# Optimization experiments

Measured on AMD Instinct MI355X. Metric: run time of the kernel, lower is better.

Reference implementation:

```python
import jax, jax.numpy as jnp
import numpy as np

CODE_DIMS = [32, 32, 16]   # prod = 16384 out features
FEAT_DIM = 1024
EPS = 1e-6


def setup_inputs() -> dict:
    key = jax.random.key(0)
    kx, kw = jax.random.split(key)
    x = jax.random.normal(kx, (4, 2048, FEAT_DIM), dtype=jnp.float32)
    # per-chunk trunc-normal init like _init_weights: std = sqrt(2/(feat_dim+code_dim)), clipped at +-3 std
    parts = []
    for i, cd in enumerate(CODE_DIMS):
        std = float(np.sqrt(2.0 / (FEAT_DIM + cd)))
        parts.append(std * jax.random.truncated_normal(
            jax.random.fold_in(kw, i), -3.0, 3.0, (cd, FEAT_DIM), dtype=jnp.float32))
    weight = jnp.concatenate(parts, axis=0)  # (sum(code_dims)=80, feat_dim)
    return {"x": x, "weight": weight}


def _rms_norm(y):
    var = jnp.mean(y * y, axis=-1, keepdims=True) + EPS
    return y * jax.lax.rsqrt(var)


def reference(x, weight):
    # split weight rows into the low-rank factors
    a, b, c = jnpp_split = jnp.split(weight, np.cumsum(CODE_DIMS)[:-1].tolist(), axis=0)
    # outer product over code dims, shared feature axis z -> dynamic weight (prod(code_dims), feat_dim)
    W = jnp.einsum('az,bz,cz->abcz', a, b, c).reshape(-1, weight.shape[-1])
    y = jnp.einsum('bsi,oi->bso', x, W)  # dense projection
    return _rms_norm(y)
```

## Files before the change

### kernel.cpp

```cpp
#include <hip/hip_runtime.h>
#include <hip/hip_bf16.h>

typedef unsigned short u16;
typedef __attribute__((ext_vector_type(8))) short bf16x8;
typedef __attribute__((ext_vector_type(4))) float f32x4;
typedef __attribute__((ext_vector_type(8))) unsigned short ushort8;

#define FEAT 1024
#define NOUT 16384
#define EPS 1e-6f
#define NT 16

#define GLOBAL_AS __attribute__((address_space(1)))
#define LDS_AS __attribute__((address_space(3)))

__device__ __forceinline__ void load16_to_lds(const u16* g, u16* l) {
    __builtin_amdgcn_global_load_lds((const GLOBAL_AS void*)g, (LDS_AS void*)l, 16, 0, 0);
}

__device__ __forceinline__ u16 f32_to_bf16_bits(float f) {
    __hip_bfloat16 h = __float2bfloat16(f);
    return *reinterpret_cast<u16*>(&h);
}

__device__ __forceinline__ float bf16_bits_to_f32(u16 b) {
    unsigned u = ((unsigned)b) << 16;
    float f;
    __builtin_memcpy(&f, &u, 4);
    return f;
}

__global__ void wbuild_kernel(const float* __restrict__ w, u16* __restrict__ Wb) {
    const int t  = blockIdx.x * 256 + threadIdx.x;
    const int p  = t >> 7;
    const int k0 = (t & 127) << 3;
    const int o  = (p & ~63) | ((p & 15) << 2) | ((p >> 4) & 3);
    const int ai = o >> 9;
    const int bi = (o >> 4) & 31;
    const int ci = o & 15;
    const float* A = w + ai * FEAT + k0;
    const float* B = w + (32 + bi) * FEAT + k0;
    const float* C = w + (64 + ci) * FEAT + k0;
    ushort8 r;
#pragma unroll
    for (int j = 0; j < 8; ++j) r[j] = f32_to_bf16_bits(A[j] * B[j] * C[j]);
    *reinterpret_cast<ushort8*>(Wb + (size_t)t * 8) = r;
}

__global__ void xcast_kernel(const float* __restrict__ x, u16* __restrict__ Xb) {
    const int t = blockIdx.x * 256 + threadIdx.x;
    const float4* xv = reinterpret_cast<const float4*>(x) + (size_t)t * 2;
    const float4 f0 = xv[0];
    const float4 f1 = xv[1];
    float vals[8] = {f0.x, f0.y, f0.z, f0.w, f1.x, f1.y, f1.z, f1.w};
    ushort8 r;
#pragma unroll
    for (int j = 0; j < 8; ++j) r[j] = f32_to_bf16_bits(vals[j]);
    *reinterpret_cast<ushort8*>(Xb + (size_t)t * 8) = r;
}


#define LDSOFF(buf, isB, kh) (((buf) << 15) + ((isB) << 14) + ((kh) << 13))

#define STAGE(isB, tt, kh, buf) do {                                          \
    const u16* g = ((isB) ? gB : gA) + (size_t)(tt) * 64 + (kh) * 32 + w * 32768; \
    u16* l = lds + LDSOFF(buf, isB, kh) + w * 1024;                           \
    load16_to_lds(g, l);                                                      \
    load16_to_lds(g + 16384, l + 512);                                        \
} while (0)

#define RD_A(dst, mi, ks, buf) dst = *reinterpret_cast<const bf16x8*>(        \
    lds + LDSOFF(buf, 0, ks) + (wm * 128 + (mi) * 16 + fr) * 32 + ((kg ^ ((fr >> 1) & 3)) << 3))
#define RD_B(dst, nj, ks, buf) dst = *reinterpret_cast<const bf16x8*>(        \
    lds + LDSOFF(buf, 1, ks) + (wn * 64 + (nj) * 16 + fr) * 32 + ((kg ^ ((fr >> 1) & 3)) << 3))

#define BAR() do {                                                            \
    __builtin_amdgcn_sched_barrier(0);                                        \
    __builtin_amdgcn_s_barrier();                                             \
    __builtin_amdgcn_sched_barrier(0);                                        \
} while (0)

#define MFMAQ(mibase) do {                                                    \
    __builtin_amdgcn_s_setprio(1);                                            \
    _Pragma("unroll")                                                         \
    for (int mi = 0; mi < 4; ++mi) {                                          \
        acc[(mibase)+mi][0] = __builtin_amdgcn_mfma_f32_16x16x32_bf16(a[mi], b[0], acc[(mibase)+mi][0], 0, 0, 0); \
        acc[(mibase)+mi][1] = __builtin_amdgcn_mfma_f32_16x16x32_bf16(a[mi], b[1], acc[(mibase)+mi][1], 0, 0, 0); \
        acc[(mibase)+mi][2] = __builtin_amdgcn_mfma_f32_16x16x32_bf16(a[mi], b[2], acc[(mibase)+mi][2], 0, 0, 0); \
        acc[(mibase)+mi][3] = __builtin_amdgcn_mfma_f32_16x16x32_bf16(a[mi], b[3], acc[(mibase)+mi][3], 0, 0, 0); \
    }                                                                         \
    __builtin_amdgcn_s_setprio(0);                                            \
} while (0)

#define WAIT_H1(t) do {                                                       \
    if ((t) == NT - 1) { asm volatile("s_waitcnt vmcnt(0)" ::: "memory"); }   \
    else               { asm volatile("s_waitcnt vmcnt(8)" ::: "memory"); }   \
} while (0)
#define WAIT_H2(t) do {                                                       \
    if ((t) < NT - 2)       { asm volatile("s_waitcnt vmcnt(8)" ::: "memory"); } \
    else if ((t) == NT - 2) { asm volatile("s_waitcnt vmcnt(4)" ::: "memory"); } \
} while (0)

#define HALF(kh, buf, doStage, stT, stKh, stBuf, WAITC) do {                  \
    RD_A(a[0], 0, kh, buf); RD_A(a[1], 1, kh, buf);                           \
    RD_A(a[2], 2, kh, buf); RD_A(a[3], 3, kh, buf);                           \
    RD_B(b[0], 0, kh, buf); RD_B(b[1], 1, kh, buf);                           \
    RD_B(b[2], 2, kh, buf); RD_B(b[3], 3, kh, buf);                           \
    if (doStage) STAGE(0, stT, stKh, stBuf);                                  \
    MFMAQ(0);                                                                 \
    RD_A(a[0], 4, kh, buf); RD_A(a[1], 5, kh, buf);                           \
    RD_A(a[2], 6, kh, buf); RD_A(a[3], 7, kh, buf);                           \
    if (doStage) STAGE(1, stT, stKh, stBuf);                                  \
    MFMAQ(4);                                                                 \
    WAITC;                                                                    \
    BAR();                                                                    \
} while (0)

#define TILE_BODY(t, buf, nbuf) do {                                          \
    HALF(0, buf, (t) < NT - 1, (t) + 1, 1, nbuf, WAIT_H1(t));                 \
    HALF(1, buf, (t) < NT - 2, (t) + 2, 0, buf,  WAIT_H2(t));                 \
} while (0)

__global__ __launch_bounds__(512, 2) void gemm_kernel(const u16* __restrict__ Xb,
                                                      const u16* __restrict__ Wb,
                                                      u16* __restrict__ Y) {
    __shared__ u16 lds[65536];

    const int tid  = threadIdx.x;
    const int lane = tid & 63;
    const int w    = tid >> 6;
    const int wm   = w >> 2;
    const int wn   = w & 3;
    const int fr   = lane & 15;
    const int kg   = lane >> 4;

    const int bid = blockIdx.x;
    const int xcd = bid & 7;
    const int o   = bid >> 3;
    const int cb  = xcd * 8 + (o >> 7) * 4 + (o & 3);
    const int rb  = (o >> 2) & 31;
    const int brow = rb * 256;
    const int bcol = cb * 256;

    const int srow   = lane >> 2;
    const int kchunk = (lane & 3) ^ ((lane >> 3) & 3);
    const u16* gA = Xb + (size_t)(brow + srow) * FEAT + kchunk * 8;
    const u16* gB = Wb + (size_t)(bcol + srow) * FEAT + kchunk * 8;

    f32x4 acc[8][4] = {};
    bf16x8 a[4], b[4];

    STAGE(0, 0, 0, 0);
    STAGE(1, 0, 0, 0);
    STAGE(0, 0, 1, 0);
    STAGE(1, 0, 1, 0);
    STAGE(0, 1, 0, 1);
    STAGE(1, 1, 0, 1);
    asm volatile("s_waitcnt vmcnt(8)" ::: "memory");
    BAR();

    for (int tt = 0; tt < NT; tt += 2) {
        TILE_BODY(tt, 0, 1);
        TILE_BODY(tt + 1, 1, 0);
    }

    const int colbase = bcol + wn * 64 + fr * 4;
#pragma unroll
    for (int mi = 0; mi < 8; ++mi) {
#pragma unroll
        for (int r = 0; r < 4; ++r) {
            const int row = brow + wm * 128 + mi * 16 + kg * 4 + r;
            const unsigned lo = (unsigned)f32_to_bf16_bits(acc[mi][0][r]) |
                                ((unsigned)f32_to_bf16_bits(acc[mi][1][r]) << 16);
            const unsigned hi = (unsigned)f32_to_bf16_bits(acc[mi][2][r]) |
                                ((unsigned)f32_to_bf16_bits(acc[mi][3][r]) << 16);
            uint2 pk; pk.x = lo; pk.y = hi;
            *reinterpret_cast<uint2*>(Y + (size_t)row * 32768 + colbase) = pk;
        }
    }
}

__global__ __launch_bounds__(1024) void scale_kernel(const u16* __restrict__ Y,
                                                     float* __restrict__ out) {
    const int row = blockIdx.x;
    const int tid = threadIdx.x;
    const ushort8* yr = reinterpret_cast<const ushort8*>(Y + (size_t)row * 32768);
    const ushort8 v0 = yr[2 * tid];
    const ushort8 v1 = yr[2 * tid + 1];

    float f[16];
#pragma unroll
    for (int j = 0; j < 8; ++j) {
        f[j]     = bf16_bits_to_f32(v0[j]);
        f[8 + j] = bf16_bits_to_f32(v1[j]);
    }
    float ss = 0.f;
#pragma unroll
    for (int j = 0; j < 16; ++j) ss += f[j] * f[j];

#pragma unroll
    for (int off = 1; off < 64; off <<= 1) ss += __shfl_xor(ss, off, 64);
    __shared__ float wss[16];
    if ((tid & 63) == 0) wss[tid >> 6] = ss;
    __syncthreads();
    float tot = 0.f;
#pragma unroll
    for (int i = 0; i < 16; ++i) tot += wss[i];
    const float sc = rsqrtf(tot * (1.0f / (float)NOUT) + EPS);

    float4* orow = reinterpret_cast<float4*>(out + (size_t)row * NOUT) + tid * 4;
#pragma unroll
    for (int q = 0; q < 4; ++q) {
        float4 ov;
        ov.x = f[q * 4 + 0] * sc;
        ov.y = f[q * 4 + 1] * sc;
        ov.z = f[q * 4 + 2] * sc;
        ov.w = f[q * 4 + 3] * sc;
        orow[q] = ov;
    }
}

extern "C" void kernel_launch(void* const* d_in, const int* in_sizes, int n_in,
                              void* d_out, int out_size, void* d_ws, size_t ws_size,
                              hipStream_t stream) {
    const float* x = (const float*)d_in[0];
    const float* w = (const float*)d_in[1];
    float* out = (float*)d_out;

    const int M = in_sizes[0] / FEAT;

    u16* Wb = (u16*)d_ws;
    u16* Xb = (u16*)((char*)d_ws + (size_t)NOUT * FEAT * 2);

    u16* Y = (u16*)d_out;

    wbuild_kernel<<<(NOUT * (FEAT / 8)) / 256, 256, 0, stream>>>(w, Wb);
    xcast_kernel<<<(M * FEAT / 8) / 256, 256, 0, stream>>>(x, Xb);

    const int nblk = (M / 256) * (NOUT / 256);
    gemm_kernel<<<nblk, 512, 0, stream>>>(Xb, Wb, Y);

    scale_kernel<<<M, 1024, 0, stream>>>(Y, out);
}
```

Baseline: 451.7 us.

## Simplify GEMM pipeline to whole-tile double buffering with one barrier per tile

Replaces the half-tile staggered prefetch schedule, which staged 32-wide K halves two steps ahead with fine-grained vmcnt waits and two barriers per tile, with a plain double-buffered scheme. Each iteration issues the full next K-tile load to LDS, then runs both K halves with all 8 A and 4 B fragments read up front before 32 MFMAs, and finishes with a full vmcnt(0) wait and one barrier. This halves the barriers and simplifies scheduling. The cost is shallower prefetch, since every tile waits for its load to drain completely, and more live registers for the fragments.

```diff
diff --git a/kernel.cpp b/kernel.cpp
--- a/kernel.cpp
+++ b/kernel.cpp
@@ -62,11 +62,21 @@
 
 #define LDSOFF(buf, isB, kh) (((buf) << 15) + ((isB) << 14) + ((kh) << 13))
 
-#define STAGE(isB, tt, kh, buf) do {                                          \
-    const u16* g = ((isB) ? gB : gA) + (size_t)(tt) * 64 + (kh) * 32 + w * 32768; \
-    u16* l = lds + LDSOFF(buf, isB, kh) + w * 1024;                           \
-    load16_to_lds(g, l);                                                      \
-    load16_to_lds(g + 16384, l + 512);                                        \
+#define STAGE_FULL(tt, buf) do {                                              \
+    const u16* gx = gA + (size_t)(tt) * 64 + (size_t)w * 32768;               \
+    const u16* gw = gB + (size_t)(tt) * 64 + (size_t)w * 32768;               \
+    u16* lx0 = lds + LDSOFF(buf, 0, 0) + w * 1024;                            \
+    u16* lx1 = lds + LDSOFF(buf, 0, 1) + w * 1024;                            \
+    u16* lw0 = lds + LDSOFF(buf, 1, 0) + w * 1024;                            \
+    u16* lw1 = lds + LDSOFF(buf, 1, 1) + w * 1024;                            \
+    load16_to_lds(gx,              lx0);                                      \
+    load16_to_lds(gx + 16384,      lx0 + 512);                                \
+    load16_to_lds(gx + 32,         lx1);                                      \
+    load16_to_lds(gx + 32 + 16384, lx1 + 512);                                \
+    load16_to_lds(gw,              lw0);                                      \
+    load16_to_lds(gw + 16384,      lw0 + 512);                                \
+    load16_to_lds(gw + 32,         lw1);                                      \
+    load16_to_lds(gw + 32 + 16384, lw1 + 512);                                \
 } while (0)
 
 #define RD_A(dst, mi, ks, buf) dst = *reinterpret_cast<const bf16x8*>(        \
@@ -80,45 +90,58 @@
     __builtin_amdgcn_sched_barrier(0);                                        \
 } while (0)
 
-#define MFMAQ(mibase) do {                                                    \
+#define HALF(kh, buf) do {                                                    \
+    bf16x8 a0, a1, a2, a3, a4, a5, a6, a7, b0, b1, b2, b3;                    \
+    RD_A(a0, 0, kh, buf); RD_A(a1, 1, kh, buf);                               \
+    RD_A(a2, 2, kh, buf); RD_A(a3, 3, kh, buf);                               \
+    RD_A(a4, 4, kh, buf); RD_A(a5, 5, kh, buf);                               \
+    RD_A(a6, 6, kh, buf); RD_A(a7, 7, kh, buf);                               \
+    RD_B(b0, 0, kh, buf); RD_B(b1, 1, kh, buf);                               \
+    RD_B(b2, 2, kh, buf); RD_B(b3, 3, kh, buf);                               \
     __builtin_amdgcn_s_setprio(1);                                            \
-    _Pragma("unroll")                                                         \
-    for (int mi = 0; mi < 4; ++mi) {                                          \
-        acc[(mibase)+mi][0] = __builtin_amdgcn_mfma_f32_16x16x32_bf16(a[mi], b[0], acc[(mibase)+mi][0], 0, 0, 0); \
-        acc[(mibase)+mi][1] = __builtin_amdgcn_mfma_f32_16x16x32_bf16(a[mi], b[1], acc[(mibase)+mi][1], 0, 0, 0); \
-        acc[(mibase)+mi][2] = __builtin_amdgcn_mfma_f32_16x16x32_bf16(a[mi], b[2], acc[(mibase)+mi][2], 0, 0, 0); \
-        acc[(mibase)+mi][3] = __builtin_amdgcn_mfma_f32_16x16x32_bf16(a[mi], b[3], acc[(mibase)+mi][3], 0, 0, 0); \
+    acc[0][0] = __builtin_amdgcn_mfma_f32_16x16x32_bf16(a0, b0, acc[0][0], 0, 0, 0); \
+    acc[0][1] = __builtin_amdgcn_mfma_f32_16x16x32_bf16(a0, b1, acc[0][1], 0, 0, 0); \
+    acc[0][2] = __builtin_amdgcn_mfma_f32_16x16x32_bf16(a0, b2, acc[0][2], 0, 0, 0); \
+    acc[0][3] = __builtin_amdgcn_mfma_f32_16x16x32_bf16(a0, b3, acc[0][3], 0, 0, 0); \
+    acc[1][0] = __builtin_amdgcn_mfma_f32_16x16x32_bf16(a1, b0, acc[1][0], 0, 0, 0); \
+    acc[1][1] = __builtin_amdgcn_mfma_f32_16x16x32_bf16(a1, b1, acc[1][1], 0, 0, 0); \
+    acc[1][2] = __builtin_amdgcn_mfma_f32_16x16x32_bf16(a1, b2, acc[1][2], 0, 0, 0); \
+    acc[1][3] = __builtin_amdgcn_mfma_f32_16x16x32_bf16(a1, b3, acc[1][3], 0, 0, 0); \
+    acc[2][0] = __builtin_amdgcn_mfma_f32_16x16x32_bf16(a2, b0, acc[2][0], 0, 0, 0); \
+    acc[2][1] = __builtin_amdgcn_mfma_f32_16x16x32_bf16(a2, b1, acc[2][1], 0, 0, 0); \
+    acc[2][2] = __builtin_amdgcn_mfma_f32_16x16x32_bf16(a2, b2, acc[2][2], 0, 0, 0); \
+    acc[2][3] = __builtin_amdgcn_mfma_f32_16x16x32_bf16(a2, b3, acc[2][3], 0, 0, 0); \
+    acc[3][0] = __builtin_amdgcn_mfma_f32_16x16x32_bf16(a3, b0, acc[3][0], 0, 0, 0); \
+    acc[3][1] = __builtin_amdgcn_mfma_f32_16x16x32_bf16(a3, b1, acc[3][1], 0, 0, 0); \
+    acc[3][2] = __builtin_amdgcn_mfma_f32_16x16x32_bf16(a3, b2, acc[3][2], 0, 0, 0); \
+    acc[3][3] = __builtin_amdgcn_mfma_f32_16x16x32_bf16(a3, b3, acc[3][3], 0, 0, 0); \
+    acc[4][0] = __builtin_amdgcn_mfma_f32_16x16x32_bf16(a4, b0, acc[4][0], 0, 0, 0); \
+    acc[4][1] = __builtin_amdgcn_mfma_f32_16x16x32_bf16(a4, b1, acc[4][1], 0, 0, 0); \
+    acc[4][2] = __builtin_amdgcn_mfma_f32_16x16x32_bf16(a4, b2, acc[4][2], 0, 0, 0); \
+    acc[4][3] = __builtin_amdgcn_mfma_f32_16x16x32_bf16(a4, b3, acc[4][3], 0, 0, 0); \
+    acc[5][0] = __builtin_amdgcn_mfma_f32_16x16x32_bf16(a5, b0, acc[5][0], 0, 0, 0); \
+    acc[5][1] = __builtin_amdgcn_mfma_f32_16x16x32_bf16(a5, b1, acc[5][1], 0, 0, 0); \
+    acc[5][2] = __builtin_amdgcn_mfma_f32_16x16x32_bf16(a5, b2, acc[5][2], 0, 0, 0); \
+    acc[5][3] = __builtin_amdgcn_mfma_f32_16x16x32_bf16(a5, b3, acc[5][3], 0, 0, 0); \
+    acc[6][0] = __builtin_amdgcn_mfma_f32_16x16x32_bf16(a6, b0, acc[6][0], 0, 0, 0); \
+    acc[6][1] = __builtin_amdgcn_mfma_f32_16x16x32_bf16(a6, b1, acc[6][1], 0, 0, 0); \
+    acc[6][2] = __builtin_amdgcn_mfma_f32_16x16x32_bf16(a6, b2, acc[6][2], 0, 0, 0); \
+    acc[6][3] = __builtin_amdgcn_mfma_f32_16x16x32_bf16(a6, b3, acc[6][3], 0, 0, 0); \
+    acc[7][0] = __builtin_amdgcn_mfma_f32_16x16x32_bf16(a7, b0, acc[7][0], 0, 0, 0); \
+    acc[7][1] = __builtin_amdgcn_mfma_f32_16x16x32_bf16(a7, b1, acc[7][1], 0, 0, 0); \
+    acc[7][2] = __builtin_amdgcn_mfma_f32_16x16x32_bf16(a7, b2, acc[7][2], 0, 0, 0); \
+    acc[7][3] = __builtin_amdgcn_mfma_f32_16x16x32_bf16(a7, b3, acc[7][3], 0, 0, 0); \
+    __builtin_amdgcn_s_setprio(0);                                            \
+} while (0)
+
+#define TILE(t, buf, nbuf) do {                                               \
+    if ((t) < NT - 1) STAGE_FULL((t) + 1, nbuf);                              \
+    HALF(0, buf);                                                             \
+    HALF(1, buf);                                                             \
+    if ((t) < NT - 1) {                                                       \
+        asm volatile("s_waitcnt vmcnt(0)" ::: "memory");                      \
+        BAR();                                                                \
     }                                                                         \
-    __builtin_amdgcn_s_setprio(0);                                            \
-} while (0)
-
-#define WAIT_H1(t) do {                                                       \
-    if ((t) == NT - 1) { asm volatile("s_waitcnt vmcnt(0)" ::: "memory"); }   \
-    else               { asm volatile("s_waitcnt vmcnt(8)" ::: "memory"); }   \
-} while (0)
-#define WAIT_H2(t) do {                                                       \
-    if ((t) < NT - 2)       { asm volatile("s_waitcnt vmcnt(8)" ::: "memory"); } \
-    else if ((t) == NT - 2) { asm volatile("s_waitcnt vmcnt(4)" ::: "memory"); } \
-} while (0)
-
-#define HALF(kh, buf, doStage, stT, stKh, stBuf, WAITC) do {                  \
-    RD_A(a[0], 0, kh, buf); RD_A(a[1], 1, kh, buf);                           \
-    RD_A(a[2], 2, kh, buf); RD_A(a[3], 3, kh, buf);                           \
-    RD_B(b[0], 0, kh, buf); RD_B(b[1], 1, kh, buf);                           \
-    RD_B(b[2], 2, kh, buf); RD_B(b[3], 3, kh, buf);                           \
-    if (doStage) STAGE(0, stT, stKh, stBuf);                                  \
-    MFMAQ(0);                                                                 \
-    RD_A(a[0], 4, kh, buf); RD_A(a[1], 5, kh, buf);                           \
-    RD_A(a[2], 6, kh, buf); RD_A(a[3], 7, kh, buf);                           \
-    if (doStage) STAGE(1, stT, stKh, stBuf);                                  \
-    MFMAQ(4);                                                                 \
-    WAITC;                                                                    \
-    BAR();                                                                    \
-} while (0)
-
-#define TILE_BODY(t, buf, nbuf) do {                                          \
-    HALF(0, buf, (t) < NT - 1, (t) + 1, 1, nbuf, WAIT_H1(t));                 \
-    HALF(1, buf, (t) < NT - 2, (t) + 2, 0, buf,  WAIT_H2(t));                 \
 } while (0)
 
 __global__ __launch_bounds__(512, 2) void gemm_kernel(const u16* __restrict__ Xb,
@@ -148,20 +171,14 @@
     const u16* gB = Wb + (size_t)(bcol + srow) * FEAT + kchunk * 8;
 
     f32x4 acc[8][4] = {};
-    bf16x8 a[4], b[4];
-
-    STAGE(0, 0, 0, 0);
-    STAGE(1, 0, 0, 0);
-    STAGE(0, 0, 1, 0);
-    STAGE(1, 0, 1, 0);
-    STAGE(0, 1, 0, 1);
-    STAGE(1, 1, 0, 1);
-    asm volatile("s_waitcnt vmcnt(8)" ::: "memory");
+
+    STAGE_FULL(0, 0);
+    asm volatile("s_waitcnt vmcnt(0)" ::: "memory");
     BAR();
 
     for (int tt = 0; tt < NT; tt += 2) {
-        TILE_BODY(tt, 0, 1);
-        TILE_BODY(tt + 1, 1, 0);
+        TILE(tt, 0, 1);
+        TILE(tt + 1, 1, 0);
     }
 
     const int colbase = bcol + wn * 64 + fr * 4;
```

New measurement: 595.9 us. 1.32x slower.
